# Kernel tuning notes

Hardware: AMD Instinct MI355X
Metric: run time of the kernel (lower is better)

Reference implementation:

```python
import jax, jax.numpy as jnp
import numpy as np

B, S, V, D = 4, 2048, 50265, 768
H_LF, DH = 12, 64          # longformer-base heads
C, W = 256, 256            # chunk size, one-sided window
DFF = 3072
NH, DK = 4, 768            # outer MultiHeadAttention(n_head=4, d_k=d_v=768)


def layer_norm(x, g, b, eps=1e-5):
    mu = jnp.mean(x, axis=-1, keepdims=True)
    var = jnp.var(x, axis=-1, keepdims=True)
    return (x - mu) * jax.lax.rsqrt(var + eps) * g + b


def _overlap_chunks(t):
    # t: [B,H,S,dh] -> [B,H,nc,3c,dh] key blocks (chunks j-1,j,j+1, zero-padded at ends)
    nc = S // C
    tp = jnp.pad(t, ((0, 0), (0, 0), (C, C), (0, 0)))
    tr = tp.reshape(t.shape[0], t.shape[1], nc + 2, C, t.shape[-1])
    return jnp.concatenate([tr[:, :, :nc], tr[:, :, 1:nc + 1], tr[:, :, 2:]], axis=3)


def sliding_window_attn(q, k, v):
    # exact band attention: query i attends keys j with |i-j| <= W
    nc = S // C
    qc = q.reshape(q.shape[0], q.shape[1], nc, C, DH)
    kb = _overlap_chunks(k)
    vb = _overlap_chunks(v)
    scores = jnp.einsum('bhncd,bhnkd->bhnck', qc, kb) / np.sqrt(DH)
    ci = jnp.arange(C)[:, None]
    ki = jnp.arange(3 * C)[None, :]
    band = jnp.abs(ki - C - ci) <= W                      # [c,3c]
    n = jnp.arange(nc)[:, None]
    kpos = n * C - C + jnp.arange(3 * C)[None, :]
    valid = (kpos >= 0) & (kpos < S)                      # [nc,3c]
    mask = band[None, :, :] & valid[:, None, :]           # [nc,c,3c]
    scores = jnp.where(mask[None, None], scores, -1e9)
    a = jax.nn.softmax(scores, axis=-1)
    out = jnp.einsum('bhnck,bhnkd->bhncd', a, vb)
    return out.reshape(q.shape)


def longformer_layer(x, emb, pos, ln_e_g, ln_e_b, lf_wq, lf_wk, lf_wv, lf_wo,
                     ln1_g, ln1_b, w1, w2, ln2_g, ln2_b):
    h = layer_norm(emb[x] + pos[None], ln_e_g, ln_e_b)    # [B,S,D]
    def heads(w):
        return (h @ w).reshape(B, S, H_LF, DH).transpose(0, 2, 1, 3)
    q, k, v = heads(lf_wq), heads(lf_wk), heads(lf_wv)
    a = sliding_window_attn(q, k, v)                      # [B,H,S,dh]
    a = a.transpose(0, 2, 1, 3).reshape(B, S, D) @ lf_wo
    h = layer_norm(h + a, ln1_g, ln1_b)
    f = jax.nn.gelu(h @ w1) @ w2
    return layer_norm(h + f, ln2_g, ln2_b)


def mha_and_pool(x, out_lf, mha_wq, mha_wk, mha_wv, mha_fc, mha_ln_g, mha_ln_b):
    residual = out_lf
    def heads(w):
        return (out_lf @ w).reshape(B, S, NH, DK).transpose(0, 2, 1, 3)
    q, k, v = heads(mha_wq), heads(mha_wk), heads(mha_wv)
    scores = jnp.einsum('bhqd,bhkd->bhqk', q, k) / np.sqrt(DK)
    key_mask = (x != 0)[:, None, None, :]
    scores = jnp.where(key_mask, scores, -1e9)
    a = jax.nn.softmax(scores, axis=-1)
    o = jnp.einsum('bhqk,bhkd->bhqd', a, v)
    o = o.transpose(0, 2, 1, 3).reshape(B, S, NH * DK) @ mha_fc
    out_attn = layer_norm(o + residual, mha_ln_g, mha_ln_b)
    return jnp.max(out_attn, axis=1)                      # max_pool1d over seq -> [B,D]


def setup_inputs() -> dict:
    key = jax.random.key(0)
    ks = jax.random.split(key, 16)
    s = 0.02
    d = {
        'x': jax.random.randint(ks[0], (B, S), 0, V),
        'emb': jax.random.normal(ks[1], (V, D), jnp.float32) * s,
        'pos': jax.random.normal(ks[2], (S, D), jnp.float32) * s,
        'ln_e_g': jnp.ones((D,), jnp.float32), 'ln_e_b': jnp.zeros((D,), jnp.float32),
        'lf_wq': jax.random.normal(ks[3], (D, D), jnp.float32) * s,
        'lf_wk': jax.random.normal(ks[4], (D, D), jnp.float32) * s,
        'lf_wv': jax.random.normal(ks[5], (D, D), jnp.float32) * s,
        'lf_wo': jax.random.normal(ks[6], (D, D), jnp.float32) * s,
        'ln1_g': jnp.ones((D,), jnp.float32), 'ln1_b': jnp.zeros((D,), jnp.float32),
        'w1': jax.random.normal(ks[7], (D, DFF), jnp.float32) * s,
        'w2': jax.random.normal(ks[8], (DFF, D), jnp.float32) * s,
        'ln2_g': jnp.ones((D,), jnp.float32), 'ln2_b': jnp.zeros((D,), jnp.float32),
        'mha_wq': jax.random.normal(ks[9], (D, NH * DK), jnp.float32) * s,
        'mha_wk': jax.random.normal(ks[10], (D, NH * DK), jnp.float32) * s,
        'mha_wv': jax.random.normal(ks[11], (D, NH * DK), jnp.float32) * s,
        'mha_fc': jax.random.normal(ks[12], (NH * DK, D), jnp.float32) * s,
        'mha_ln_g': jnp.ones((D,), jnp.float32), 'mha_ln_b': jnp.zeros((D,), jnp.float32),
    }
    return d


def reference(x, emb, pos, ln_e_g, ln_e_b, lf_wq, lf_wk, lf_wv, lf_wo,
              ln1_g, ln1_b, w1, w2, ln2_g, ln2_b,
              mha_wq, mha_wk, mha_wv, mha_fc, mha_ln_g, mha_ln_b):
    out_lf = longformer_layer(x, emb, pos, ln_e_g, ln_e_b, lf_wq, lf_wk, lf_wv, lf_wo,
                              ln1_g, ln1_b, w1, w2, ln2_g, ln2_b)
    out_lf = jax.lax.stop_gradient(out_lf)  # torch.no_grad() around longformer
    return mha_and_pool(x, out_lf, mha_wq, mha_wk, mha_wv, mha_fc, mha_ln_g, mha_ln_b)
```

## Files before the change

### kernel.cpp

```cpp
#include <hip/hip_runtime.h>
#include <hip/hip_bf16.h>
#include <math.h>

#define DEV static __device__ __forceinline__

typedef unsigned short u16;
typedef __attribute__((ext_vector_type(8))) __bf16 bf16x8;
typedef __attribute__((ext_vector_type(8))) unsigned short u16x8;
typedef __attribute__((ext_vector_type(4))) float f32x4;
typedef __attribute__((ext_vector_type(4))) int i32x4;

constexpr int SL  = 2048;
constexpr int DM  = 768;
constexpr int CC  = 256;
constexpr int DH  = 64;
constexpr int DFF = 3072;
constexpr int DKM = 768;

DEV float b2f(u16 u){ union{float f; unsigned u;} c; c.u = ((unsigned)u)<<16; return c.f; }
DEV u16 f2b(float f){ union{float f; unsigned u;} c; c.f=f; unsigned r=(c.u + 0x7fffu + ((c.u>>16)&1u))>>16; return (u16)r; }

DEV void gld16(u16* lds, const u16* g){
  __builtin_amdgcn_global_load_lds((const __attribute__((address_space(1))) void*)g,
                                   (__attribute__((address_space(3))) void*)lds, 16, 0, 0);
}

DEV float wred_sum(float v){
#pragma unroll
  for (int o=32;o;o>>=1) v += __shfl_xor(v,o,64);
  return v;
}
DEV float wred_max(float v){
#pragma unroll
  for (int o=32;o;o>>=1) v = fmaxf(v, __shfl_xor(v,o,64));
  return v;
}
DEV float bred_sum(float v, float* sm){
  v = wred_sum(v);
  if ((threadIdx.x & 63)==0) sm[threadIdx.x>>6] = v;
  __syncthreads();
  float r = sm[0]+sm[1]+sm[2]+sm[3];
  __syncthreads();
  return r;
}

#define PHASE_SYNC \
  __builtin_amdgcn_s_barrier(); \
  asm volatile("s_waitcnt lgkmcnt(0)" ::: "memory"); \
  __builtin_amdgcn_sched_barrier(0); \
  __builtin_amdgcn_s_setprio(1);
#define PHASE_END \
  __builtin_amdgcn_s_setprio(0); \
  __builtin_amdgcn_s_barrier();

#define MFMA_PH(MH, NH) \
  { _Pragma("unroll") for (int mi2=0; mi2<4; ++mi2) { \
      _Pragma("unroll") for (int ni2=0; ni2<2; ++ni2) { \
        acc[(MH)*4+mi2][(NH)*2+ni2] = __builtin_amdgcn_mfma_f32_16x16x32_bf16(Af[mi2][0], Bf[(NH)*2+ni2][0], acc[(MH)*4+mi2][(NH)*2+ni2], 0,0,0); \
        acc[(MH)*4+mi2][(NH)*2+ni2] = __builtin_amdgcn_mfma_f32_16x16x32_bf16(Af[mi2][1], Bf[(NH)*2+ni2][1], acc[(MH)*4+mi2][(NH)*2+ni2], 0,0,0); } } }

template<int MODE, int EPI>
__global__ __launch_bounds__(512,2) void gemm256_k(
    const u16* __restrict__ A, const u16* __restrict__ Bt,
    float* __restrict__ Cf, u16* __restrict__ Cb,
    u16* __restrict__ Cb2, u16* __restrict__ Cb3,
    int K, int lda, int ldb, int ldc)
{
  extern __shared__ u16 lds_dyn[];
  const int tid = threadIdx.x, lane = tid & 63, wv = tid >> 6;
  const int wr = wv >> 2, wc = wv & 3;
  const int m0 = blockIdx.x * 256, n0 = blockIdx.y * 256, z = blockIdx.z;
  const int nt = K >> 6;

  int bb = 0, hh = 0;
  long long baseA = 0, baseB = 0;
  if constexpr (MODE==1) { bb=z>>2; hh=z&3; baseA=(long long)bb*SL*3072 + hh*DKM; baseB=baseA; }

  const int rb = (wv*64 + lane) >> 3;
  const int sg = ((lane & 7) ^ (rb & 7)) * 8;
  const int rd0 = (lane & 15)*64 + (((lane>>4) ^ (lane & 7)) * 8);
  const int rd1 = rd0 ^ 32;

  auto stageA = [&](int buf, int half, int kt) {
#pragma unroll
    for (int tt = 0; tt < 2; ++tt) {
      const int t = half + tt*2;
      gld16(lds_dyn + buf*16384 + t*4096 + wv*512,
            A + baseA + (long long)(m0 + t*64 + rb)*lda + (long long)kt*64 + sg);
    }
  };
  auto stageB = [&](int buf, int half, int kt) {
#pragma unroll
    for (int tt = 0; tt < 2; ++tt) {
      const int t = half*2 + tt;
      gld16(lds_dyn + 32768 + buf*16384 + t*4096 + wv*512,
            Bt + baseB + (long long)(n0 + t*64 + rb)*ldb + (long long)kt*64 + sg);
    }
  };

  f32x4 acc[8][4] = {};
  bf16x8 Af[4][2];
  bf16x8 Bf[4][2];

  stageA(0,0,0); stageB(0,0,0); stageB(0,1,0); stageA(0,1,0);
  stageA(1,0,1); stageB(1,0,1); stageB(1,1,1);
  asm volatile("s_waitcnt vmcnt(6)" ::: "memory");
  __builtin_amdgcn_s_barrier();

  for (int t = 0; t < nt; ++t) {
    const int d = t & 1;
    const u16* As_d = lds_dyn + d*16384;
    const u16* Bs_d = lds_dyn + 32768 + d*16384;
#pragma unroll
    for (int mi2=0; mi2<4; ++mi2) {
      const u16* p = As_d + (wr*128 + mi2*16)*64;
      Af[mi2][0] = *(const bf16x8*)(p + rd0);
      Af[mi2][1] = *(const bf16x8*)(p + rd1);
    }
#pragma unroll
    for (int ni2=0; ni2<2; ++ni2) {
      const u16* p = Bs_d + (wc*64 + ni2*16)*64;
      Bf[ni2][0] = *(const bf16x8*)(p + rd0);
      Bf[ni2][1] = *(const bf16x8*)(p + rd1);
    }
    if (t+1 < nt) stageA(d^1, 1, t+1);
    PHASE_SYNC; MFMA_PH(0,0); PHASE_END;
#pragma unroll
    for (int ni2=0; ni2<2; ++ni2) {
      const u16* p = Bs_d + (wc*64 + 32 + ni2*16)*64;
      Bf[2+ni2][0] = *(const bf16x8*)(p + rd0);
      Bf[2+ni2][1] = *(const bf16x8*)(p + rd1);
    }
    if (t+2 < nt) stageA(d, 0, t+2);
    PHASE_SYNC; MFMA_PH(0,1); PHASE_END;
#pragma unroll
    for (int mi2=0; mi2<4; ++mi2) {
      const u16* p = As_d + (wr*128 + 64 + mi2*16)*64;
      Af[mi2][0] = *(const bf16x8*)(p + rd0);
      Af[mi2][1] = *(const bf16x8*)(p + rd1);
    }
    if (t+2 < nt) stageB(d, 0, t+2);
    PHASE_SYNC; MFMA_PH(1,0); PHASE_END;
    if (t+2 < nt) stageB(d, 1, t+2);
    __builtin_amdgcn_s_barrier();
    __builtin_amdgcn_s_setprio(1);
    MFMA_PH(1,1);
    __builtin_amdgcn_s_setprio(0);
    if (t+2 < nt)      { asm volatile("s_waitcnt vmcnt(6)" ::: "memory"); }
    else if (t+1 < nt) { asm volatile("s_waitcnt vmcnt(0)" ::: "memory"); }
    __builtin_amdgcn_s_barrier();
  }

#pragma unroll
  for (int mi=0; mi<8; ++mi)
#pragma unroll
  for (int ni=0; ni<4; ++ni)
#pragma unroll
  for (int r=0; r<4; ++r) {
    int m = m0 + wr*128 + mi*16 + ((lane>>4)<<2) + r;
    int n = n0 + wc*64  + ni*16 + (lane & 15);
    float v = acc[mi][ni][r];
    if constexpr (EPI==2) {
      float u = 0.7978845608f*(v + 0.044715f*v*v*v);
      float th = 1.f - 2.f/(__expf(2.f*u)+1.f);
      v = 0.5f*v*(1.f + th);
    }
    if constexpr (EPI==3) v *= 0.0360843918f;
    if constexpr (MODE==3) {
      int seg = n / 3072, nn = n - seg*3072;
      u16* dst = seg==0 ? Cb : (seg==1 ? Cb2 : Cb3);
      dst[(long long)m*3072 + nn] = f2b(v);
    } else {
      long long ci;
      if constexpr (MODE==1) ci = (long long)z*SL*SL + (long long)m*SL + n;
      else                   ci = (long long)m*ldc + n;
      if constexpr (EPI==0) Cf[ci] = v; else Cb[ci] = f2b(v);
    }
  }
}

#define MFMA_Q(MB, NB, AF) \
  { _Pragma("unroll") for (int mi2=0; mi2<2; ++mi2) { \
      _Pragma("unroll") for (int ni2=0; ni2<2; ++ni2) { \
        acc[(MB)+mi2][(NB)+ni2] = __builtin_amdgcn_mfma_f32_16x16x32_bf16(AF[mi2][0], Bf[(NB)+ni2][0], acc[(MB)+mi2][(NB)+ni2], 0,0,0); \
        acc[(MB)+mi2][(NB)+ni2] = __builtin_amdgcn_mfma_f32_16x16x32_bf16(AF[mi2][1], Bf[(NB)+ni2][1], acc[(MB)+mi2][(NB)+ni2], 0,0,0); } } }

__global__ __launch_bounds__(512,2) void gemm128n_k(
    const u16* __restrict__ A, const u16* __restrict__ Bt, u16* __restrict__ Cb, int K)
{
  extern __shared__ u16 lds_dyn[];
  const int tid = threadIdx.x, lane = tid & 63, wv = tid >> 6;
  const int wr = wv >> 1, wc = wv & 1;
  const int m0 = blockIdx.x * 256, n0 = blockIdx.y * 128, z = blockIdx.z;
  const int bb = z >> 2, hh = z & 3;
  const long long baseA = (long long)z*SL*SL;
  const long long baseB = ((long long)bb*3072 + hh*DKM)*SL;
  const int nt = K >> 6;

  const int rb = (wv*64 + lane) >> 3;
  const int sg = ((lane & 7) ^ (rb & 7)) * 8;
  const int rd0 = (lane & 15)*64 + (((lane>>4) ^ (lane & 7)) * 8);
  const int rd1 = rd0 ^ 32;

  auto stageA = [&](int buf, int half, int kt) {
#pragma unroll
    for (int tt = 0; tt < 2; ++tt) {
      const int t = half*2 + tt;
      gld16(lds_dyn + buf*16384 + t*4096 + wv*512,
            A + baseA + (long long)(m0 + t*64 + rb)*SL + (long long)kt*64 + sg);
    }
  };
  auto stageB = [&](int buf, int idx, int kt) {
    gld16(lds_dyn + 32768 + buf*8192 + idx*4096 + wv*512,
          Bt + baseB + (long long)(n0 + idx*64 + rb)*SL + (long long)kt*64 + sg);
  };

  f32x4 acc[4][4] = {};
  bf16x8 Af[2][2];
  bf16x8 Bf[4][2];

  stageA(0,0,0); stageB(0,0,0); stageB(0,1,0); stageA(0,1,0);
  stageA(1,0,1); stageB(1,0,1); stageB(1,1,1);
  asm volatile("s_waitcnt vmcnt(4)" ::: "memory");
  __builtin_amdgcn_s_barrier();

  for (int t = 0; t < nt; ++t) {
    const int d = t & 1;
    const u16* As_d = lds_dyn + d*16384;
    const u16* Bs_d = lds_dyn + 32768 + d*8192;
#pragma unroll
    for (int mi2=0; mi2<2; ++mi2) {
      const u16* p = As_d + (wr*32 + mi2*16)*64;
      Af[mi2][0] = *(const bf16x8*)(p + rd0);
      Af[mi2][1] = *(const bf16x8*)(p + rd1);
    }
#pragma unroll
    for (int ni2=0; ni2<2; ++ni2) {
      const u16* p = Bs_d + (wc*64 + ni2*16)*64;
      Bf[ni2][0] = *(const bf16x8*)(p + rd0);
      Bf[ni2][1] = *(const bf16x8*)(p + rd1);
    }
    if (t+1 < nt) stageA(d^1, 1, t+1);
    PHASE_SYNC; MFMA_Q(0,0,Af); PHASE_END;
#pragma unroll
    for (int ni2=0; ni2<2; ++ni2) {
      const u16* p = Bs_d + (wc*64 + 32 + ni2*16)*64;
      Bf[2+ni2][0] = *(const bf16x8*)(p + rd0);
      Bf[2+ni2][1] = *(const bf16x8*)(p + rd1);
    }
    if (t+2 < nt) stageA(d, 0, t+2);
    PHASE_SYNC; MFMA_Q(0,2,Af); PHASE_END;
#pragma unroll
    for (int mi2=0; mi2<2; ++mi2) {
      const u16* p = As_d + (128 + wr*32 + mi2*16)*64;
      Af[mi2][0] = *(const bf16x8*)(p + rd0);
      Af[mi2][1] = *(const bf16x8*)(p + rd1);
    }
    if (t+2 < nt) stageB(d, 0, t+2);
    PHASE_SYNC; MFMA_Q(2,0,Af); PHASE_END;
    if (t+2 < nt) stageB(d, 1, t+2);
    __builtin_amdgcn_s_barrier();
    __builtin_amdgcn_s_setprio(1);
    MFMA_Q(2,2,Af);
    __builtin_amdgcn_s_setprio(0);
    if (t+2 < nt)      { asm volatile("s_waitcnt vmcnt(4)" ::: "memory"); }
    else if (t+1 < nt) { asm volatile("s_waitcnt vmcnt(0)" ::: "memory"); }
    __builtin_amdgcn_s_barrier();
  }

#pragma unroll
  for (int mi=0; mi<4; ++mi)
#pragma unroll
  for (int ni=0; ni<4; ++ni)
#pragma unroll
  for (int r=0; r<4; ++r) {
    int m = m0 + (mi>>1)*128 + wr*32 + (mi&1)*16 + ((lane>>4)<<2) + r;
    int n = n0 + wc*64 + ni*16 + (lane & 15);
    Cb[((long long)bb*SL + m)*3072 + hh*DKM + n] = f2b(acc[mi][ni][r]);
  }
}

template<int BM, int BN, int MODE, int EPI>
__global__ __launch_bounds__(256) void gemm_k(
    const u16* __restrict__ A, const u16* __restrict__ Bt,
    float* __restrict__ Cf, u16* __restrict__ Cb,
    u16* __restrict__ Cb2, u16* __restrict__ Cb3,
    int K, int lda, int ldb, int ldc)
{
  constexpr int BK = 32;
  constexpr int WM = BM/2, WN = BN/2, FM = WM/16, FN = WN/16;
  __shared__ __attribute__((aligned(16))) u16 As[BM*BK];
  __shared__ __attribute__((aligned(16))) u16 Bs[BN*BK];
  const int tid = threadIdx.x, lane = tid & 63, wv = tid >> 6;
  const int wr = wv >> 1, wc = wv & 1;
  const int m0 = blockIdx.x * BM, n0 = blockIdx.y * BN;

  f32x4 acc[FM][FN] = {};

  for (int kt = 0; kt < K; kt += BK) {
#pragma unroll
    for (int t = 0; t < (BM*4)/256; ++t) {
      int cb  = (t*4 + wv)*64;
      int ch  = cb + lane;
      int row = ch >> 2, cp = ch & 3;
      int gp  = cp ^ (row & 3) ^ ((row >> 2) & 1);
      long long ga = (long long)(m0 + row)*lda + (kt + gp*8);
      gld16(&As[cb*8], A + ga);
    }
#pragma unroll
    for (int t = 0; t < (BN*4)/256; ++t) {
      int cb  = (t*4 + wv)*64;
      int ch  = cb + lane;
      int row = ch >> 2, cp = ch & 3;
      int gp  = cp ^ (row & 3) ^ ((row >> 2) & 1);
      long long gb = (long long)(n0 + row)*ldb + (kt + gp*8);
      gld16(&Bs[cb*8], Bt + gb);
    }
    __syncthreads();
    bf16x8 af[FM], bfr[FN];
#pragma unroll
    for (int mi=0; mi<FM; ++mi) {
      int row = wr*WM + mi*16 + (lane & 15);
      int cp  = (lane >> 4) ^ (row & 3) ^ ((row >> 2) & 1);
      af[mi] = *reinterpret_cast<const bf16x8*>(&As[row*BK + cp*8]);
    }
#pragma unroll
    for (int ni=0; ni<FN; ++ni) {
      int row = wc*WN + ni*16 + (lane & 15);
      int cp  = (lane >> 4) ^ (row & 3) ^ ((row >> 2) & 1);
      bfr[ni] = *reinterpret_cast<const bf16x8*>(&Bs[row*BK + cp*8]);
    }
#pragma unroll
    for (int mi=0; mi<FM; ++mi)
#pragma unroll
      for (int ni=0; ni<FN; ++ni)
        acc[mi][ni] = __builtin_amdgcn_mfma_f32_16x16x32_bf16(af[mi], bfr[ni], acc[mi][ni], 0,0,0);
    __syncthreads();
  }

#pragma unroll
  for (int mi=0; mi<FM; ++mi)
#pragma unroll
  for (int ni=0; ni<FN; ++ni)
#pragma unroll
  for (int r=0; r<4; ++r) {
    int m = m0 + wr*WM + mi*16 + ((lane>>4)<<2) + r;
    int n = n0 + wc*WN + ni*16 + (lane & 15);
    float v = acc[mi][ni][r];
    if constexpr (MODE==5) {
      int seg = n / 768, nn = n - seg*768;
      u16* dst = seg==0 ? Cb : (seg==1 ? Cb2 : Cb3);
      dst[(long long)m*768 + nn] = f2b(v);
    } else {
      long long ci = (long long)m*ldc + n;
      if constexpr (EPI==0) Cf[ci] = v; else Cb[ci] = f2b(v);
    }
  }
}

__global__ __launch_bounds__(256) void sw_attn_k(
    const u16* __restrict__ Qm, const u16* __restrict__ Km,
    const u16* __restrict__ Vt, u16* __restrict__ Om)
{
  __shared__ __attribute__((aligned(16))) u16 Kb_s[64*64];
  __shared__ __attribute__((aligned(16))) u16 Vb_s[64*64];
  __shared__ __attribute__((aligned(16))) u16 Pb_s[4*32*64];
  const int tid = threadIdx.x, lane = tid & 63, wv = tid >> 6;
  const int qc = blockIdx.x >> 1, half = blockIdx.x & 1;
  const int h = blockIdx.y, b = blockIdx.z;
  const int q0 = qc*256 + half*128 + wv*32;
  const long long rowbase = (long long)b*SL;

  bf16x8 Qf[2][2];
#pragma unroll
  for (int mi=0;mi<2;++mi)
#pragma unroll
    for (int ks=0;ks<2;++ks)
      Qf[mi][ks] = *(const bf16x8*)(Qm + (rowbase + q0 + mi*16 + (lane&15))*DM + h*DH + ks*32 + (lane>>4)*8);

  f32x4 accO[2][4] = {};
  float mrun[2][4], lrun[2][4];
#pragma unroll
  for (int mi=0;mi<2;++mi)
#pragma unroll
    for (int r=0;r<4;++r){ mrun[mi][r]=-3e38f; lrun[mi][r]=0.f; }

  const int srow = tid >> 3;
  const int schunk = (tid & 7) ^ (srow & 7);

  const int kb0 = qc*256 + half*128 - 256;
  const int slo = kb0 < 0 ? ((-kb0) >> 6) : 0;
  const int shi_t = (SL - kb0) >> 6;
  const int shi = shi_t < 10 ? shi_t : 10;

  const int qpb = q0 + ((lane>>4)<<2);

  for (int s = slo; s < shi; ++s) {
    const int kb = kb0 + s*64;
#pragma unroll
    for (int ii=0; ii<2; ++ii) {
      gld16(Kb_s + ii*2048 + wv*512,
            Km + (rowbase + kb + srow + ii*32)*DM + h*DH + schunk*8);
      gld16(Vb_s + ii*2048 + wv*512,
            Vt + ((long long)b*DM + h*DH + srow + ii*32)*SL + kb + schunk*8);
    }
    asm volatile("s_waitcnt vmcnt(0)" ::: "memory");
    __syncthreads();

    f32x4 accS[2][4] = {};
    {
      bf16x8 Kf[4][2];
#pragma unroll
      for (int nf=0;nf<4;++nf){
        int row = nf*16 + (lane&15);
#pragma unroll
        for (int ks=0;ks<2;++ks){
          int ch = ((lane>>4) + ks*4) ^ (row&7);
          Kf[nf][ks] = *(const bf16x8*)(Kb_s + row*64 + ch*8);
        }
      }
#pragma unroll
      for (int mi=0;mi<2;++mi)
#pragma unroll
        for (int nf=0;nf<4;++nf){
          accS[mi][nf] = __builtin_amdgcn_mfma_f32_16x16x32_bf16(Qf[mi][0], Kf[nf][0], accS[mi][nf], 0,0,0);
          accS[mi][nf] = __builtin_amdgcn_mfma_f32_16x16x32_bf16(Qf[mi][1], Kf[nf][1], accS[mi][nf], 0,0,0);
        }
    }

    float smax[2][4];
#pragma unroll
    for (int mi=0;mi<2;++mi)
#pragma unroll
      for (int r=0;r<4;++r) smax[mi][r] = -3e38f;
#pragma unroll
    for (int mi=0;mi<2;++mi)
#pragma unroll
      for (int nf=0;nf<4;++nf)
#pragma unroll
        for (int r=0;r<4;++r){
          int dd = (kb + nf*16 + (lane&15)) - (qpb + mi*16 + r);
          bool ok = (dd <= 256) && (dd >= -256);
          float v = ok ? accS[mi][nf][r]*0.125f : -3e38f;
          accS[mi][nf][r] = v;
          smax[mi][r] = fmaxf(smax[mi][r], v);
        }
#pragma unroll
    for (int mi=0;mi<2;++mi)
#pragma unroll
      for (int r=0;r<4;++r){
        float v = smax[mi][r];
        v = fmaxf(v, __shfl_xor(v,1,64)); v = fmaxf(v, __shfl_xor(v,2,64));
        v = fmaxf(v, __shfl_xor(v,4,64)); v = fmaxf(v, __shfl_xor(v,8,64));
        smax[mi][r] = v;
      }

#pragma unroll
    for (int mi=0;mi<2;++mi)
#pragma unroll
      for (int r=0;r<4;++r){
        float mn = fmaxf(mrun[mi][r], smax[mi][r]);
        float sc = __expf(mrun[mi][r] - mn);
        float ls = 0.f;
#pragma unroll
        for (int nf=0;nf<4;++nf){
          float sv = accS[mi][nf][r];
          float p = (sv > -1e37f) ? __expf(sv - mn) : 0.f;
          accS[mi][nf][r] = p;
          ls += p;
        }
        ls += __shfl_xor(ls,1,64); ls += __shfl_xor(ls,2,64);
        ls += __shfl_xor(ls,4,64); ls += __shfl_xor(ls,8,64);
        lrun[mi][r] = lrun[mi][r]*sc + ls;
        mrun[mi][r] = mn;
#pragma unroll
        for (int df=0;df<4;++df) accO[mi][df][r] *= sc;
      }
#pragma unroll
    for (int mi=0;mi<2;++mi)
#pragma unroll
      for (int nf=0;nf<4;++nf)
#pragma unroll
        for (int r=0;r<4;++r){
          int ql = mi*16 + ((lane>>4)<<2) + r;
          int k  = nf*16 + (lane&15);
          int ch = (k>>3) ^ (ql&7);
          Pb_s[wv*2048 + ql*64 + ch*8 + (k&7)] = f2b(accS[mi][nf][r]);
        }
    asm volatile("s_waitcnt lgkmcnt(0)" ::: "memory");
    __builtin_amdgcn_sched_barrier(0);

    {
      bf16x8 Pf[2][2], Vf[4][2];
#pragma unroll
      for (int mi=0;mi<2;++mi){
        int ql = mi*16 + (lane&15);
#pragma unroll
        for (int ks=0;ks<2;++ks){
          int ch = ((lane>>4) + ks*4) ^ (ql&7);
          Pf[mi][ks] = *(const bf16x8*)(Pb_s + wv*2048 + ql*64 + ch*8);
        }
      }
#pragma unroll
      for (int df=0;df<4;++df){
        int dr = df*16 + (lane&15);
#pragma unroll
        for (int ks=0;ks<2;++ks){
          int ch = ((lane>>4) + ks*4) ^ (dr&7);
          Vf[df][ks] = *(const bf16x8*)(Vb_s + dr*64 + ch*8);
        }
      }
#pragma unroll
      for (int mi=0;mi<2;++mi)
#pragma unroll
        for (int df=0;df<4;++df){
          accO[mi][df] = __builtin_amdgcn_mfma_f32_16x16x32_bf16(Pf[mi][0], Vf[df][0], accO[mi][df], 0,0,0);
          accO[mi][df] = __builtin_amdgcn_mfma_f32_16x16x32_bf16(Pf[mi][1], Vf[df][1], accO[mi][df], 0,0,0);
        }
    }
    __syncthreads();
  }

#pragma unroll
  for (int mi=0;mi<2;++mi)
#pragma unroll
    for (int df=0;df<4;++df)
#pragma unroll
      for (int r=0;r<4;++r){
        long long row = rowbase + qpb + mi*16 + r;
        int col = h*DH + df*16 + (lane&15);
        Om[row*DM + col] = f2b(accO[mi][df][r] / lrun[mi][r]);
      }
}

__global__ __launch_bounds__(256) void embed_ln_k(const int* __restrict__ x,
    const float* __restrict__ emb, const float* __restrict__ pos,
    const float* __restrict__ g, const float* __restrict__ bta,
    float* __restrict__ of, u16* __restrict__ ob)
{
  __shared__ float sm[4];
  const int row = blockIdx.x, s = row & (SL-1);
  const long long tok = x[row];
  const float* e = emb + tok*DM;
  const float* p = pos + (long long)s*DM;
  float v[3], su=0.f, sq=0.f;
#pragma unroll
  for (int i=0;i<3;++i){ int d=threadIdx.x+i*256; v[i]=e[d]+p[d]; su+=v[i]; sq+=v[i]*v[i]; }
  su = bred_sum(su, sm); sq = bred_sum(sq, sm);
  float mean = su*(1.f/DM), var = sq*(1.f/DM)-mean*mean, rs = rsqrtf(var+1e-5f);
#pragma unroll
  for (int i=0;i<3;++i){ int d=threadIdx.x+i*256;
    float o = (v[i]-mean)*rs*g[d] + bta[d];
    of[(long long)row*DM+d]=o; ob[(long long)row*DM+d]=f2b(o); }
}

__global__ __launch_bounds__(256) void resid_ln_k(const float* __restrict__ a, const float* __restrict__ c,
    const float* __restrict__ g, const float* __restrict__ bta,
    float* __restrict__ of, u16* __restrict__ ob)
{
  __shared__ float sm[4];
  const long long row = blockIdx.x;
  const float* ra = a + row*DM;
  const float* rc = c + row*DM;
  float v[3], su=0.f, sq=0.f;
#pragma unroll
  for (int i=0;i<3;++i){ int d=threadIdx.x+i*256; v[i]=ra[d]+rc[d]; su+=v[i]; sq+=v[i]*v[i]; }
  su = bred_sum(su, sm); sq = bred_sum(sq, sm);
  float mean = su*(1.f/DM), var = sq*(1.f/DM)-mean*mean, rs = rsqrtf(var+1e-5f);
#pragma unroll
  for (int i=0;i<3;++i){ int d=threadIdx.x+i*256;
    float o = (v[i]-mean)*rs*g[d] + bta[d];
    of[row*DM+d]=o; if (ob) ob[row*DM+d]=f2b(o); }
}

__global__ __launch_bounds__(256) void transp_w_k(const float* __restrict__ W, u16* __restrict__ Wt, int Kd, int Nd)
{
  __shared__ float t[32][33];
  int n0 = blockIdx.x*32, k0 = blockIdx.y*32;
  int lx = threadIdx.x & 31, ly = threadIdx.x >> 5;
#pragma unroll
  for (int i=0;i<4;++i) t[ly+i*8][lx] = W[(long long)(k0+ly+i*8)*Nd + n0+lx];
  __syncthreads();
#pragma unroll
  for (int i=0;i<4;++i) Wt[(long long)(n0+ly+i*8)*Kd + k0+lx] = f2b(t[lx][ly+i*8]);
}

__global__ __launch_bounds__(256) void transp_b_k(const u16* __restrict__ in, u16* __restrict__ out, int Nc)
{
  __shared__ u16 t[32][33];
  int c0 = blockIdx.x*32, r0 = blockIdx.y*32;
  int lx = threadIdx.x & 31, ly = threadIdx.x >> 5;
#pragma unroll
  for (int i=0;i<4;++i) t[ly+i*8][lx] = in[(long long)(r0+ly+i*8)*Nc + c0+lx];
  __syncthreads();
  int b = r0 >> 11, s0 = r0 & (SL-1);
#pragma unroll
  for (int i=0;i<4;++i) out[((long long)b*Nc + c0+ly+i*8)*SL + s0+lx] = t[lx][ly+i*8];
}

__global__ __launch_bounds__(256) void mha_softmax_k(u16* __restrict__ sc, const int* __restrict__ x)
{
  const int r = blockIdx.x*4 + (threadIdx.x >> 6);
  const int lane = threadIdx.x & 63;
  const int z = r >> 11;
  const int b = z >> 2;
  u16* row = sc + (long long)z*SL*SL + (long long)(r & (SL-1))*SL;
  const int* xb = x + b*SL;
  float v[32]; float mx = -3e38f;
#pragma unroll
  for (int i=0;i<4;++i){
    const int j0 = i*512 + lane*8;
    u16x8 pv = *(const u16x8*)(row + j0);
    i32x4 xa = *(const i32x4*)(xb + j0);
    i32x4 xc = *(const i32x4*)(xb + j0 + 4);
#pragma unroll
    for (int e=0;e<8;++e){
      int xv = e<4 ? xa[e] : xc[e-4];
      float f = (xv != 0) ? b2f(pv[e]) : -3e38f;
      v[i*8+e] = f;
      mx = fmaxf(mx, f);
    }
  }
  mx = wred_max(mx);
  float s = 0.f;
#pragma unroll
  for (int i=0;i<32;++i){ v[i] = (v[i] > -1e37f) ? __expf(v[i]-mx) : 0.f; s += v[i]; }
  s = wred_sum(s);
  float inv = 1.f/s;
#pragma unroll
  for (int i=0;i<4;++i){
    u16x8 ov;
#pragma unroll
    for (int e=0;e<8;++e) ov[e] = f2b(v[i*8+e]*inv);
    *(u16x8*)(row + i*512 + lane*8) = ov;
  }
}

__global__ __launch_bounds__(256) void pool_part_k(const float* __restrict__ f, float* __restrict__ pp)
{
  int b = blockIdx.x, ch = blockIdx.y;
  float m0=-3e38f, m1=-3e38f, m2=-3e38f;
  for (int s = ch*128; s < ch*128+128; ++s){
    const float* r = f + ((long long)b*SL + s)*DM;
    m0=fmaxf(m0,r[threadIdx.x]); m1=fmaxf(m1,r[threadIdx.x+256]); m2=fmaxf(m2,r[threadIdx.x+512]);
  }
  float* o = pp + (long long)(b*16+ch)*DM;
  o[threadIdx.x]=m0; o[threadIdx.x+256]=m1; o[threadIdx.x+512]=m2;
}

__global__ __launch_bounds__(256) void pool_red_k(const float* __restrict__ pp, float* __restrict__ out)
{
  int b = blockIdx.x;
#pragma unroll
  for (int i=0;i<3;++i){
    int d = threadIdx.x + i*256;
    float m = -3e38f;
    for (int c=0;c<16;++c) m = fmaxf(m, pp[(long long)(b*16+c)*DM + d]);
    out[(long long)b*DM + d] = m;
  }
}

extern "C" void kernel_launch(void* const* d_in, const int* in_sizes, int n_in,
                              void* d_out, int out_size, void* d_ws, size_t ws_size,
                              hipStream_t stream)
{
  const int*   x      = (const int*)  d_in[0];
  const float* emb    = (const float*)d_in[1];
  const float* pos    = (const float*)d_in[2];
  const float* ln_e_g = (const float*)d_in[3];
  const float* ln_e_b = (const float*)d_in[4];
  const float* lf_wq  = (const float*)d_in[5];
  const float* lf_wk  = (const float*)d_in[6];
  const float* lf_wv  = (const float*)d_in[7];
  const float* lf_wo  = (const float*)d_in[8];
  const float* ln1_g  = (const float*)d_in[9];
  const float* ln1_b  = (const float*)d_in[10];
  const float* w1     = (const float*)d_in[11];
  const float* w2     = (const float*)d_in[12];
  const float* ln2_g  = (const float*)d_in[13];
  const float* ln2_b  = (const float*)d_in[14];
  const float* mha_wq = (const float*)d_in[15];
  const float* mha_wk = (const float*)d_in[16];
  const float* mha_wv = (const float*)d_in[17];
  const float* mha_fc = (const float*)d_in[18];
  const float* mha_ln_g = (const float*)d_in[19];
  const float* mha_ln_b = (const float*)d_in[20];

  (void)hipFuncSetAttribute((const void*)gemm256_k<0,2>, hipFuncAttributeMaxDynamicSharedMemorySize, 131072);
  (void)hipFuncSetAttribute((const void*)gemm256_k<1,3>, hipFuncAttributeMaxDynamicSharedMemorySize, 131072);
  (void)hipFuncSetAttribute((const void*)gemm256_k<3,1>, hipFuncAttributeMaxDynamicSharedMemorySize, 131072);
  (void)hipFuncSetAttribute((const void*)gemm128n_k,     hipFuncAttributeMaxDynamicSharedMemorySize, 98304);

  const long long R = 8192;
  float* F0 = (float*)d_ws;
  float* F1 = F0 + R*DM;
  float* F2 = F1 + R*DM;
  u16* B0 = (u16*)(F2 + R*DM);
  u16* B1 = B0 + R*DM;
  u16* B2 = B1 + R*DM;
  u16* B3 = B2 + R*DM;
  u16* WT = B3 + R*DM;
  u16* G1 = WT + (long long)9216*DM;
  u16* G2 = G1 + R*DFF;
  u16* G3 = G2 + R*DFF;
  u16* SC = G3 + R*DFF;
  float* PP = (float*)(SC + (long long)16*SL*SL);

  dim3 T(256), T5(512);
  const size_t SM256 = 131072, SM128 = 98304;

  embed_ln_k<<<dim3(8192), T, 0, stream>>>(x, emb, pos, ln_e_g, ln_e_b, F0, B0);

  transp_w_k<<<dim3(24,24), T, 0, stream>>>(lf_wq, WT,               DM, DM);
  transp_w_k<<<dim3(24,24), T, 0, stream>>>(lf_wk, WT + 768*768,     DM, DM);
  transp_w_k<<<dim3(24,24), T, 0, stream>>>(lf_wv, WT + 2*768*768,   DM, DM);
  gemm_k<128,128,5,1><<<dim3(64,18), T, 0, stream>>>(B0, WT, nullptr, B1, B2, SC, DM, DM, DM, 0);
  transp_b_k<<<dim3(24,256), T, 0, stream>>>(SC, B3, DM);

  sw_attn_k<<<dim3(16,12,4), T, 0, stream>>>(B1, B2, B3, B0);

  transp_w_k<<<dim3(24,24), T, 0, stream>>>(lf_wo, WT, DM, DM);
  gemm_k<128,128,0,0><<<dim3(64,6), T, 0, stream>>>(B0, WT, F1, nullptr, nullptr, nullptr, DM, DM, DM, DM);
  resid_ln_k<<<dim3(8192), T, 0, stream>>>(F0, F1, ln1_g, ln1_b, F2, B1);

  transp_w_k<<<dim3(96,24), T, 0, stream>>>(w1, WT, DM, DFF);
  gemm256_k<0,2><<<dim3(32,12,1), T5, SM256, stream>>>(B1, WT, nullptr, G1, nullptr, nullptr, DM, DM, DM, DFF);
  transp_w_k<<<dim3(24,96), T, 0, stream>>>(w2, WT, DFF, DM);
  gemm_k<128,128,0,0><<<dim3(64,6), T, 0, stream>>>(G1, WT, F1, nullptr, nullptr, nullptr, DFF, DFF, DFF, DM);
  resid_ln_k<<<dim3(8192), T, 0, stream>>>(F2, F1, ln2_g, ln2_b, F0, B2);

  transp_w_k<<<dim3(96,24), T, 0, stream>>>(mha_wq, WT,                 DM, DFF);
  transp_w_k<<<dim3(96,24), T, 0, stream>>>(mha_wk, WT + (long long)3072*768, DM, DFF);
  transp_w_k<<<dim3(96,24), T, 0, stream>>>(mha_wv, WT + (long long)6144*768, DM, DFF);
  gemm256_k<3,1><<<dim3(32,36,1), T5, SM256, stream>>>(B2, WT, nullptr, G1, G2, SC, DM, DM, DM, 0);
  transp_b_k<<<dim3(96,256), T, 0, stream>>>(SC, G3, DFF);

  gemm256_k<1,3><<<dim3(8,8,16), T5, SM256, stream>>>(G1, G2, nullptr, SC, nullptr, nullptr, DKM, 3072, 3072, 0);
  mha_softmax_k<<<dim3(8192), T, 0, stream>>>(SC, x);
  gemm128n_k<<<dim3(8,6,16), T5, SM128, stream>>>(SC, G3, G2, SL);

  transp_w_k<<<dim3(24,96), T, 0, stream>>>(mha_fc, WT, DFF, DM);
  gemm_k<128,128,0,0><<<dim3(64,6), T, 0, stream>>>(G2, WT, F1, nullptr, nullptr, nullptr, DFF, DFF, DFF, DM);
  resid_ln_k<<<dim3(8192), T, 0, stream>>>(F0, F1, mha_ln_g, mha_ln_b, F2, nullptr);

  pool_part_k<<<dim3(4,16), T, 0, stream>>>(F2, PP);
  pool_red_k<<<dim3(4), T, 0, stream>>>(PP, (float*)d_out);
}
```

Measured before the change: 926.6 us.

## Split-K the N=768 GEMMs, vectorize weight transpose, widen pooling grid

The three output-projection GEMMs with N=768 (384 blocks) now run split-K by two over blockIdx.z. Each half writes fp32 partials to the scores scratch buffer, and the residual-layernorm kernel sums the two partials. This doubles the block count on the 256-CU device, at the cost of extra fp32 partial traffic. The weight transpose kernel moves to 64x64 tiles with float4 loads and 4-wide bf16 stores, and the max-pool partial stage uses 64 chunks instead of 16 to get more parallelism.

After: 936.2 us. No clear change (+1.0%).

```diff
diff --git a/kernel.cpp b/kernel.cpp
--- a/kernel.cpp
+++ b/kernel.cpp
@@ -7,12 +7,12 @@
 typedef unsigned short u16;
 typedef __attribute__((ext_vector_type(8))) __bf16 bf16x8;
 typedef __attribute__((ext_vector_type(8))) unsigned short u16x8;
+typedef __attribute__((ext_vector_type(4))) unsigned short u16x4;
 typedef __attribute__((ext_vector_type(4))) float f32x4;
 typedef __attribute__((ext_vector_type(4))) int i32x4;
 
 constexpr int SL  = 2048;
 constexpr int DM  = 768;
-constexpr int CC  = 256;
 constexpr int DH  = 64;
 constexpr int DFF = 3072;
 constexpr int DKM = 768;
@@ -293,11 +293,14 @@
   __shared__ __attribute__((aligned(16))) u16 Bs[BN*BK];
   const int tid = threadIdx.x, lane = tid & 63, wv = tid >> 6;
   const int wr = wv >> 1, wc = wv & 1;
-  const int m0 = blockIdx.x * BM, n0 = blockIdx.y * BN;
+  const int m0 = blockIdx.x * BM, n0 = blockIdx.y * BN, z = blockIdx.z;
+
+  int k_lo = 0, k_hi = K;
+  if constexpr (MODE==6) { int kh = K >> 1; k_lo = z*kh; k_hi = k_lo + kh; }
 
   f32x4 acc[FM][FN] = {};
 
-  for (int kt = 0; kt < K; kt += BK) {
+  for (int kt = k_lo; kt < k_hi; kt += BK) {
 #pragma unroll
     for (int t = 0; t < (BM*4)/256; ++t) {
       int cb  = (t*4 + wv)*64;
@@ -351,6 +354,8 @@
       int seg = n / 768, nn = n - seg*768;
       u16* dst = seg==0 ? Cb : (seg==1 ? Cb2 : Cb3);
       dst[(long long)m*768 + nn] = f2b(v);
+    } else if constexpr (MODE==6) {
+      Cf[(long long)z*8192*ldc + (long long)m*ldc + n] = v;
     } else {
       long long ci = (long long)m*ldc + n;
       if constexpr (EPI==0) Cf[ci] = v; else Cb[ci] = f2b(v);
@@ -555,6 +560,7 @@
 }
 
 __global__ __launch_bounds__(256) void resid_ln_k(const float* __restrict__ a, const float* __restrict__ c,
+    const float* __restrict__ c2,
     const float* __restrict__ g, const float* __restrict__ bta,
     float* __restrict__ of, u16* __restrict__ ob)
 {
@@ -564,7 +570,12 @@
   const float* rc = c + row*DM;
   float v[3], su=0.f, sq=0.f;
 #pragma unroll
-  for (int i=0;i<3;++i){ int d=threadIdx.x+i*256; v[i]=ra[d]+rc[d]; su+=v[i]; sq+=v[i]*v[i]; }
+  for (int i=0;i<3;++i){
+    int d=threadIdx.x+i*256;
+    v[i]=ra[d]+rc[d];
+    if (c2) v[i]+=c2[row*DM+d];
+    su+=v[i]; sq+=v[i]*v[i];
+  }
   su = bred_sum(su, sm); sq = bred_sum(sq, sm);
   float mean = su*(1.f/DM), var = sq*(1.f/DM)-mean*mean, rs = rsqrtf(var+1e-5f);
 #pragma unroll
@@ -575,14 +586,21 @@
 
 __global__ __launch_bounds__(256) void transp_w_k(const float* __restrict__ W, u16* __restrict__ Wt, int Kd, int Nd)
 {
-  __shared__ float t[32][33];
-  int n0 = blockIdx.x*32, k0 = blockIdx.y*32;
-  int lx = threadIdx.x & 31, ly = threadIdx.x >> 5;
-#pragma unroll
-  for (int i=0;i<4;++i) t[ly+i*8][lx] = W[(long long)(k0+ly+i*8)*Nd + n0+lx];
+  __shared__ float t[64][65];
+  int n0 = blockIdx.x*64, k0 = blockIdx.y*64;
+  int lx = threadIdx.x & 15, ly = threadIdx.x >> 4;
+#pragma unroll
+  for (int i=0;i<4;++i){
+    const float4 v = *(const float4*)(W + (long long)(k0+ly+i*16)*Nd + n0 + lx*4);
+    t[ly+i*16][lx*4+0]=v.x; t[ly+i*16][lx*4+1]=v.y; t[ly+i*16][lx*4+2]=v.z; t[ly+i*16][lx*4+3]=v.w;
+  }
   __syncthreads();
 #pragma unroll
-  for (int i=0;i<4;++i) Wt[(long long)(n0+ly+i*8)*Kd + k0+lx] = f2b(t[lx][ly+i*8]);
+  for (int i=0;i<4;++i){
+    int nn = ly + i*16, kk = lx*4;
+    u16x4 o = { f2b(t[kk][nn]), f2b(t[kk+1][nn]), f2b(t[kk+2][nn]), f2b(t[kk+3][nn]) };
+    *(u16x4*)(Wt + (long long)(n0+nn)*Kd + k0 + kk) = o;
+  }
 }
 
 __global__ __launch_bounds__(256) void transp_b_k(const u16* __restrict__ in, u16* __restrict__ out, int Nc)
@@ -640,11 +658,11 @@
 {
   int b = blockIdx.x, ch = blockIdx.y;
   float m0=-3e38f, m1=-3e38f, m2=-3e38f;
-  for (int s = ch*128; s < ch*128+128; ++s){
+  for (int s = ch*32; s < ch*32+32; ++s){
     const float* r = f + ((long long)b*SL + s)*DM;
     m0=fmaxf(m0,r[threadIdx.x]); m1=fmaxf(m1,r[threadIdx.x+256]); m2=fmaxf(m2,r[threadIdx.x+512]);
   }
-  float* o = pp + (long long)(b*16+ch)*DM;
+  float* o = pp + (long long)(b*64+ch)*DM;
   o[threadIdx.x]=m0; o[threadIdx.x+256]=m1; o[threadIdx.x+512]=m2;
 }
 
@@ -655,7 +673,7 @@
   for (int i=0;i<3;++i){
     int d = threadIdx.x + i*256;
     float m = -3e38f;
-    for (int c=0;c<16;++c) m = fmaxf(m, pp[(long long)(b*16+c)*DM + d]);
+    for (int c=0;c<64;++c) m = fmaxf(m, pp[(long long)(b*64+c)*DM + d]);
     out[(long long)b*DM + d] = m;
   }
 }
@@ -704,6 +722,7 @@
   u16* G2 = G1 + R*DFF;
   u16* G3 = G2 + R*DFF;
   u16* SC = G3 + R*DFF;
+  float* FS = (float*)SC;
   float* PP = (float*)(SC + (long long)16*SL*SL);
 
   dim3 T(256), T5(512);
@@ -711,27 +730,27 @@
 
   embed_ln_k<<<dim3(8192), T, 0, stream>>>(x, emb, pos, ln_e_g, ln_e_b, F0, B0);
 
-  transp_w_k<<<dim3(24,24), T, 0, stream>>>(lf_wq, WT,               DM, DM);
-  transp_w_k<<<dim3(24,24), T, 0, stream>>>(lf_wk, WT + 768*768,     DM, DM);
-  transp_w_k<<<dim3(24,24), T, 0, stream>>>(lf_wv, WT + 2*768*768,   DM, DM);
+  transp_w_k<<<dim3(12,12), T, 0, stream>>>(lf_wq, WT,               DM, DM);
+  transp_w_k<<<dim3(12,12), T, 0, stream>>>(lf_wk, WT + 768*768,     DM, DM);
+  transp_w_k<<<dim3(12,12), T, 0, stream>>>(lf_wv, WT + 2*768*768,   DM, DM);
   gemm_k<128,128,5,1><<<dim3(64,18), T, 0, stream>>>(B0, WT, nullptr, B1, B2, SC, DM, DM, DM, 0);
   transp_b_k<<<dim3(24,256), T, 0, stream>>>(SC, B3, DM);
 
   sw_attn_k<<<dim3(16,12,4), T, 0, stream>>>(B1, B2, B3, B0);
 
-  transp_w_k<<<dim3(24,24), T, 0, stream>>>(lf_wo, WT, DM, DM);
-  gemm_k<128,128,0,0><<<dim3(64,6), T, 0, stream>>>(B0, WT, F1, nullptr, nullptr, nullptr, DM, DM, DM, DM);
-  resid_ln_k<<<dim3(8192), T, 0, stream>>>(F0, F1, ln1_g, ln1_b, F2, B1);
-
-  transp_w_k<<<dim3(96,24), T, 0, stream>>>(w1, WT, DM, DFF);
+  transp_w_k<<<dim3(12,12), T, 0, stream>>>(lf_wo, WT, DM, DM);
+  gemm_k<128,128,6,0><<<dim3(64,6,2), T, 0, stream>>>(B0, WT, FS, nullptr, nullptr, nullptr, DM, DM, DM, DM);
+  resid_ln_k<<<dim3(8192), T, 0, stream>>>(F0, FS, FS + R*DM, ln1_g, ln1_b, F2, B1);
+
+  transp_w_k<<<dim3(48,12), T, 0, stream>>>(w1, WT, DM, DFF);
   gemm256_k<0,2><<<dim3(32,12,1), T5, SM256, stream>>>(B1, WT, nullptr, G1, nullptr, nullptr, DM, DM, DM, DFF);
-  transp_w_k<<<dim3(24,96), T, 0, stream>>>(w2, WT, DFF, DM);
-  gemm_k<128,128,0,0><<<dim3(64,6), T, 0, stream>>>(G1, WT, F1, nullptr, nullptr, nullptr, DFF, DFF, DFF, DM);
-  resid_ln_k<<<dim3(8192), T, 0, stream>>>(F2, F1, ln2_g, ln2_b, F0, B2);
-
-  transp_w_k<<<dim3(96,24), T, 0, stream>>>(mha_wq, WT,                 DM, DFF);
-  transp_w_k<<<dim3(96,24), T, 0, stream>>>(mha_wk, WT + (long long)3072*768, DM, DFF);
-  transp_w_k<<<dim3(96,24), T, 0, stream>>>(mha_wv, WT + (long long)6144*768, DM, DFF);
+  transp_w_k<<<dim3(12,48), T, 0, stream>>>(w2, WT, DFF, DM);
+  gemm_k<128,128,6,0><<<dim3(64,6,2), T, 0, stream>>>(G1, WT, FS, nullptr, nullptr, nullptr, DFF, DFF, DFF, DM);
+  resid_ln_k<<<dim3(8192), T, 0, stream>>>(F2, FS, FS + R*DM, ln2_g, ln2_b, F0, B2);
+
+  transp_w_k<<<dim3(48,12), T, 0, stream>>>(mha_wq, WT,                 DM, DFF);
+  transp_w_k<<<dim3(48,12), T, 0, stream>>>(mha_wk, WT + (long long)3072*768, DM, DFF);
+  transp_w_k<<<dim3(48,12), T, 0, stream>>>(mha_wv, WT + (long long)6144*768, DM, DFF);
   gemm256_k<3,1><<<dim3(32,36,1), T5, SM256, stream>>>(B2, WT, nullptr, G1, G2, SC, DM, DM, DM, 0);
   transp_b_k<<<dim3(96,256), T, 0, stream>>>(SC, G3, DFF);
 
@@ -739,10 +758,10 @@
   mha_softmax_k<<<dim3(8192), T, 0, stream>>>(SC, x);
   gemm128n_k<<<dim3(8,6,16), T5, SM128, stream>>>(SC, G3, G2, SL);
 
-  transp_w_k<<<dim3(24,96), T, 0, stream>>>(mha_fc, WT, DFF, DM);
-  gemm_k<128,128,0,0><<<dim3(64,6), T, 0, stream>>>(G2, WT, F1, nullptr, nullptr, nullptr, DFF, DFF, DFF, DM);
-  resid_ln_k<<<dim3(8192), T, 0, stream>>>(F0, F1, mha_ln_g, mha_ln_b, F2, nullptr);
-
-  pool_part_k<<<dim3(4,16), T, 0, stream>>>(F2, PP);
+  transp_w_k<<<dim3(12,48), T, 0, stream>>>(mha_fc, WT, DFF, DM);
+  gemm_k<128,128,6,0><<<dim3(64,6,2), T, 0, stream>>>(G2, WT, FS, nullptr, nullptr, nullptr, DFF, DFF, DFF, DM);
+  resid_ln_k<<<dim3(8192), T, 0, stream>>>(F0, FS, FS + R*DM, mha_ln_g, mha_ln_b, F2, nullptr);
+
+  pool_part_k<<<dim3(4,64), T, 0, stream>>>(F2, PP);
   pool_red_k<<<dim3(4), T, 0, stream>>>(PP, (float*)d_out);
 }
```
